# Kernel optimization log

Measured on AMD Instinct MI355X. Metric: run time of the kernel, lower is better.

## Reference

```python
import jax, jax.numpy as jnp
import numpy as np

N = 100000   # active voxels
K = 27       # 3x3x3 kernel offsets
C = 64       # in_channels == out_channels (residual block)
EPS = 1e-5


def setup_inputs() -> dict:
    key = jax.random.key(0)
    ks = jax.random.split(key, 10)
    feats = jax.random.normal(ks[0], (N, C), dtype=jnp.float32)
    # kernel-map: for each voxel, index of the neighbor voxel for each of the 27 offsets
    nbr = jax.random.randint(ks[1], (N, K), 0, N)
    nbr = nbr.at[:, K // 2].set(jnp.arange(N))  # center offset is identity
    w_scale = 1.0 / np.sqrt(K * C)
    W1 = jax.random.normal(ks[2], (K, C, C), dtype=jnp.float32) * w_scale
    b1 = jax.random.normal(ks[3], (C,), dtype=jnp.float32) * 0.01
    g1 = jnp.ones((C,), jnp.float32)
    be1 = jnp.zeros((C,), jnp.float32)
    W2 = jax.random.normal(ks[4], (K, C, C), dtype=jnp.float32) * w_scale
    b2 = jax.random.normal(ks[5], (C,), dtype=jnp.float32) * 0.01
    g2 = jnp.ones((C,), jnp.float32)
    be2 = jnp.zeros((C,), jnp.float32)
    return {"feats": feats, "nbr": nbr, "W1": W1, "b1": b1, "g1": g1, "be1": be1,
            "W2": W2, "b2": b2, "g2": g2, "be2": be2}


def _sparse_conv(f, nbr, W, b):
    # gather neighbor features per kernel offset: [N, K, C]
    g = f[nbr]
    # per-offset matmul and reduce over offsets (gather-matmul-scatter form)
    return jnp.einsum('nkc,kcd->nd', g, W) + b


def _bn(x, gamma, beta):
    # BatchNorm over active voxels (training-mode batch stats, per channel)
    mu = x.mean(axis=0)
    var = x.var(axis=0)
    return (x - mu) * jax.lax.rsqrt(var + EPS) * gamma + beta


def reference(feats, nbr, W1, b1, g1, be1, W2, b2, g2, be2):
    h = jax.nn.relu(_bn(_sparse_conv(feats, nbr, W1, b1), g1, be1))
    h = _bn(_sparse_conv(h, nbr, W2, b2), g2, be2)
    return jax.nn.relu(h + feats)  # residual add + ReLU
```

## Files before the change

### kernel.cpp

```cpp
#include <hip/hip_runtime.h>

#define NCH 64
#define KOFF 27
#define EPSV 1e-5f

typedef __attribute__((ext_vector_type(8))) short  bf16x8;
typedef __attribute__((ext_vector_type(4))) float  f32x4;
typedef __attribute__((ext_vector_type(8))) unsigned short u16x8;

__device__ __forceinline__ unsigned short f2bf(float x) {
    unsigned int u = __float_as_uint(x);
    u += 0x7fffu + ((u >> 16) & 1u);
    return (unsigned short)(u >> 16);
}

__global__ __launch_bounds__(256)
void prep_kernel(const float* __restrict__ feats,
                 const float* __restrict__ W1, const float* __restrict__ W2,
                 unsigned short* __restrict__ fbf,
                 unsigned short* __restrict__ wt1, unsigned short* __restrict__ wt2,
                 float* __restrict__ stat, int total8)
{
    const int b = blockIdx.x;
    if (b == 0) {
        stat[threadIdx.x] = 0.f;
        return;
    }
    if (b <= 108) {
        const float* W = (b <= 54) ? W1 : W2;
        unsigned short* Wt = (b <= 54) ? wt1 : wt2;
        const int t = (b <= 54 ? b - 1 : b - 55) * 256 + threadIdx.x;
        const int l  = t & 63;
        const int ct = (t >> 6) & 3;
        const int s  = (t >> 8) & 1;
        const int k  = t >> 9;
        const int d     = ct * 16 + (l & 15);
        const int cbase = s * 32 + (l >> 4) * 8;
        u16x8 o;
#pragma unroll
        for (int j = 0; j < 8; ++j)
            o[j] = f2bf(W[(size_t)k * 4096 + (size_t)(cbase + j) * 64 + d]);
        reinterpret_cast<u16x8*>(Wt)[t] = o;
        return;
    }
    const int idx = (b - 109) * 256 + threadIdx.x;
    if (idx >= total8) return;
    const float4* xp = reinterpret_cast<const float4*>(feats) + (size_t)idx * 2;
    const float4 a = xp[0], c = xp[1];
    u16x8 o;
    o[0] = f2bf(a.x); o[1] = f2bf(a.y); o[2] = f2bf(a.z); o[3] = f2bf(a.w);
    o[4] = f2bf(c.x); o[5] = f2bf(c.y); o[6] = f2bf(c.z); o[7] = f2bf(c.w);
    reinterpret_cast<u16x8*>(fbf)[idx] = o;
}

__global__ __launch_bounds__(128, 4)
void conv_mfma_kernel(const unsigned short* __restrict__ fin,
                      const int* __restrict__ nbr,
                      const unsigned short* __restrict__ Wt,
                      const float* __restrict__ bias,
                      float* __restrict__ out, float* __restrict__ pstat, int N)
{
    __shared__ int   s_idx[32 * KOFF];
    __shared__ f32x4 s_comb4[8][64];

    const int lane = threadIdx.x & 63;
    const int wv   = threadIdx.x >> 6;
    const int n0   = blockIdx.x * 32;
    const int m    = lane & 15;
    const int quad = lane >> 4;

    {
        const int rem  = N - n0;
        const int maxi = (rem < 32 ? rem : 32) * KOFF;
        const int* nb  = nbr + (size_t)n0 * KOFF;
        for (int p = threadIdx.x; p < 32 * KOFF; p += 128)
            s_idx[p] = ((p < maxi) ? nb[p] : 0) * (NCH * 2);
    }
    __syncthreads();

    f32x4 acc[2][4];
#pragma unroll
    for (int mt = 0; mt < 2; ++mt)
#pragma unroll
        for (int ct = 0; ct < 4; ++ct) acc[mt][ct] = (f32x4){0.f, 0.f, 0.f, 0.f};

    bf16x8 A[2][2][2];
    bf16x8 B[2][4];
    const char* finB = (const char*)fin;

#define LOADA(kk, p)                                                         \
    {                                                                        \
        _Pragma("unroll")                                                    \
        for (int mt = 0; mt < 2; ++mt) {                                     \
            const int ofs = s_idx[(mt * 16 + m) * KOFF + (kk)];              \
            const char* fp = finB + ofs + quad * 16;                         \
            A[p][mt][0] = *reinterpret_cast<const bf16x8*>(fp);              \
            A[p][mt][1] = *reinterpret_cast<const bf16x8*>(fp + 64);         \
        }                                                                    \
    }

#define LOADB(kk)                                                            \
    {                                                                        \
        const unsigned short* wp = Wt + (size_t)(kk) * 4096 + lane * 8;      \
        _Pragma("unroll")                                                    \
        for (int s = 0; s < 2; ++s)                                          \
            _Pragma("unroll")                                                \
            for (int ct = 0; ct < 4; ++ct)                                   \
                B[s][ct] =                                                   \
                    *reinterpret_cast<const bf16x8*>(wp + (s * 4 + ct) * 512);\
    }

#define DOMFMA(p)                                                            \
    {                                                                        \
        _Pragma("unroll")                                                    \
        for (int mt = 0; mt < 2; ++mt)                                       \
            _Pragma("unroll")                                                \
            for (int s = 0; s < 2; ++s)                                      \
                _Pragma("unroll")                                            \
                for (int ct = 0; ct < 4; ++ct)                               \
                    acc[mt][ct] = __builtin_amdgcn_mfma_f32_16x16x32_bf16(   \
                        A[p][mt][s], B[s][ct], acc[mt][ct], 0, 0, 0);        \
    }

    const int kbeg = wv ? 14 : 0;
    const int kend = wv ? KOFF : 14;
    LOADA(kbeg, 0);
    int k = kbeg;
#pragma unroll 1
    for (; k + 2 < kend; k += 2) {
        LOADB(k);
        LOADA(k + 1, 1);
        __builtin_amdgcn_sched_barrier(0);
        DOMFMA(0);
        LOADB(k + 1);
        LOADA(k + 2, 0);
        __builtin_amdgcn_sched_barrier(0);
        DOMFMA(1);
    }
    if (k + 1 < kend) {
        LOADB(k);
        LOADA(k + 1, 1);
        __builtin_amdgcn_sched_barrier(0);
        DOMFMA(0);
        LOADB(k + 1);
        DOMFMA(1);
    } else {
        LOADB(k);
        DOMFMA(0);
    }
#undef LOADA
#undef LOADB
#undef DOMFMA

    if (wv == 1) {
#pragma unroll
        for (int mt = 0; mt < 2; ++mt)
#pragma unroll
            for (int ct = 0; ct < 4; ++ct)
                s_comb4[mt * 4 + ct][lane] = acc[mt][ct];
    }
    __syncthreads();
    if (wv == 0) {
#pragma unroll
        for (int ct = 0; ct < 4; ++ct) {
            const int ch = ct * 16 + m;
            const float bv = bias[ch];
            float s = 0.f, q = 0.f;
#pragma unroll
            for (int mt = 0; mt < 2; ++mt) {
                const f32x4 part = s_comb4[mt * 4 + ct][lane];
#pragma unroll
                for (int r = 0; r < 4; ++r) {
                    const int vox = n0 + mt * 16 + quad * 4 + r;
                    if (vox < N) {
                        const float v = acc[mt][ct][r] + part[r] + bv;
                        out[(size_t)vox * NCH + ch] = v;
                        s += v;
                        q += v * v;
                    }
                }
            }
            s += __shfl_xor(s, 16, 64);
            s += __shfl_xor(s, 32, 64);
            q += __shfl_xor(q, 16, 64);
            q += __shfl_xor(q, 32, 64);
            if (quad == 0) {
                float* pr = pstat + (size_t)blockIdx.x * 128;
                pr[ch]      = s;
                pr[64 + ch] = q;
            }
        }
    }
}

__global__ __launch_bounds__(256)
void reduce_stats_kernel(const float* __restrict__ pstat, float* __restrict__ stat,
                         int rows)
{
    __shared__ float s_[256];
    const int ch = threadIdx.x & 127;
    const int h  = threadIdx.x >> 7;
    float acc = 0.f;
    for (int r = blockIdx.x * 2 + h; r < rows; r += gridDim.x * 2)
        acc += pstat[(size_t)r * 128 + ch];
    s_[threadIdx.x] = acc;
    __syncthreads();
    if (threadIdx.x < 128)
        atomicAdd(&stat[threadIdx.x], s_[threadIdx.x] + s_[threadIdx.x + 128]);
}

__global__ __launch_bounds__(256)
void bn_relu_bf16_kernel(const float* __restrict__ x, const float* __restrict__ sums,
                         const float* __restrict__ gmm, const float* __restrict__ bet,
                         float invN, unsigned short* __restrict__ y, int total8)
{
    const int idx = blockIdx.x * 256 + threadIdx.x;
    if (idx >= total8) return;
    const int c0 = (idx & 7) * 8;
    const float4* xp = reinterpret_cast<const float4*>(x) + (size_t)idx * 2;
    const float4 a = xp[0], b = xp[1];
    float v[8] = {a.x, a.y, a.z, a.w, b.x, b.y, b.z, b.w};
    u16x8 o;
#pragma unroll
    for (int i = 0; i < 8; ++i) {
        const int c = c0 + i;
        const float mu  = sums[c] * invN;
        const float var = sums[64 + c] * invN - mu * mu;
        const float rs  = rsqrtf(var + EPSV);
        const float sc  = gmm[c] * rs;
        const float sh  = bet[c] - mu * sc;
        o[i] = f2bf(fmaxf(fmaf(v[i], sc, sh), 0.f));
    }
    reinterpret_cast<u16x8*>(y)[idx] = o;
}

__global__ __launch_bounds__(256)
void bn_res_relu_kernel(float* __restrict__ x, const float* __restrict__ feats,
                        const float* __restrict__ sums, const float* __restrict__ gmm,
                        const float* __restrict__ bet, float invN, int total4)
{
    const int idx = blockIdx.x * blockDim.x + threadIdx.x;
    if (idx >= total4) return;
    float4 v = reinterpret_cast<float4*>(x)[idx];
    const float4 f = reinterpret_cast<const float4*>(feats)[idx];
    const int c0 = (idx & 15) * 4;
    float sc[4], sh[4];
#pragma unroll
    for (int i = 0; i < 4; ++i) {
        const int c = c0 + i;
        const float mu  = sums[c] * invN;
        const float var = sums[64 + c] * invN - mu * mu;
        const float rs  = rsqrtf(var + EPSV);
        sc[i] = gmm[c] * rs;
        sh[i] = bet[c] - mu * sc[i];
    }
    v.x = fmaxf(fmaf(v.x, sc[0], sh[0]) + f.x, 0.f);
    v.y = fmaxf(fmaf(v.y, sc[1], sh[1]) + f.y, 0.f);
    v.z = fmaxf(fmaf(v.z, sc[2], sh[2]) + f.z, 0.f);
    v.w = fmaxf(fmaf(v.w, sc[3], sh[3]) + f.w, 0.f);
    reinterpret_cast<float4*>(x)[idx] = v;
}

extern "C" void kernel_launch(void* const* d_in, const int* in_sizes, int n_in,
                              void* d_out, int out_size, void* d_ws, size_t ws_size,
                              hipStream_t stream)
{
    const float* feats = (const float*)d_in[0];
    const int*   nbr   = (const int*)d_in[1];
    const float* W1    = (const float*)d_in[2];
    const float* b1    = (const float*)d_in[3];
    const float* g1    = (const float*)d_in[4];
    const float* be1   = (const float*)d_in[5];
    const float* W2    = (const float*)d_in[6];
    const float* b2    = (const float*)d_in[7];
    const float* g2    = (const float*)d_in[8];
    const float* be2   = (const float*)d_in[9];
    float* out = (float*)d_out;

    const int N  = in_sizes[0] / NCH;
    const int NC = N * NCH;
    const float invN = 1.0f / (float)N;

    float*          h0   = (float*)d_ws;
    unsigned short* fbf  = (unsigned short*)(h0 + NC);
    unsigned short* hbf  = fbf + NC;
    unsigned short* wt1  = hbf + NC;
    unsigned short* wt2  = wt1 + KOFF * 4096;
    float*          stat = (float*)(wt2 + KOFF * 4096);

    const int total8   = NC / 8;
    const int castGrid = (total8 + 255) / 256;
    const int prepGrid = 1 + 108 + castGrid;
    const int convGrid = (N + 31) / 32;

    float* pstat1 = out;
    float* pstat2 = h0;

    prep_kernel<<<prepGrid, 256, 0, stream>>>(feats, W1, W2, fbf, wt1, wt2,
                                              stat, total8);
    conv_mfma_kernel<<<convGrid, 128, 0, stream>>>(fbf, nbr, wt1, b1, h0,
                                                   pstat1, N);
    reduce_stats_kernel<<<32, 256, 0, stream>>>(pstat1, stat, convGrid);
    bn_relu_bf16_kernel<<<castGrid, 256, 0, stream>>>(h0, stat, g1, be1, invN,
                                                      hbf, total8);
    conv_mfma_kernel<<<convGrid, 128, 0, stream>>>(hbf, nbr, wt2, b2, out,
                                                   pstat2, N);
    reduce_stats_kernel<<<32, 256, 0, stream>>>(pstat2, stat + 128, convGrid);
    bn_res_relu_kernel<<<(NC / 4 + 255) / 256, 256, 0, stream>>>(
        out, feats, stat + 128, g2, be2, invN, NC / 4);
}
```

Before: 292.0 us.

## Stage conv weights in LDS and widen blocks to 128 voxels

The conv kernel now runs 4 waves per block, each owning 32 voxels across all 27 offsets, instead of 2 waves splitting the offsets for 32 voxels. Weights are staged into shared memory in chunks of 6 offsets, so all waves share them rather than each reading them from global memory. This also removes the cross-wave partial-sum combine through LDS. In exchange it adds block-wide barriers per chunk, a larger LDS footprint (about 62 KB) that limits occupancy, and more stat rows for the reduce kernel.

```diff
diff --git a/kernel.cpp b/kernel.cpp
--- a/kernel.cpp
+++ b/kernel.cpp
@@ -53,30 +53,29 @@
     reinterpret_cast<u16x8*>(fbf)[idx] = o;
 }
 
-__global__ __launch_bounds__(128, 4)
+__global__ __launch_bounds__(256, 2)
 void conv_mfma_kernel(const unsigned short* __restrict__ fin,
                       const int* __restrict__ nbr,
                       const unsigned short* __restrict__ Wt,
                       const float* __restrict__ bias,
                       float* __restrict__ out, float* __restrict__ pstat, int N)
 {
-    __shared__ int   s_idx[32 * KOFF];
-    __shared__ f32x4 s_comb4[8][64];
+    __shared__ int            s_idx[128 * KOFF];
+    __shared__ unsigned short s_w[6 * 4096];
 
     const int lane = threadIdx.x & 63;
     const int wv   = threadIdx.x >> 6;
-    const int n0   = blockIdx.x * 32;
+    const int n0   = blockIdx.x * 128;
     const int m    = lane & 15;
     const int quad = lane >> 4;
 
     {
         const int rem  = N - n0;
-        const int maxi = (rem < 32 ? rem : 32) * KOFF;
+        const int maxi = (rem < 128 ? rem : 128) * KOFF;
         const int* nb  = nbr + (size_t)n0 * KOFF;
-        for (int p = threadIdx.x; p < 32 * KOFF; p += 128)
+        for (int p = threadIdx.x; p < 128 * KOFF; p += 256)
             s_idx[p] = ((p < maxi) ? nb[p] : 0) * (NCH * 2);
     }
-    __syncthreads();
 
     f32x4 acc[2][4];
 #pragma unroll
@@ -87,21 +86,22 @@
     bf16x8 A[2][2][2];
     bf16x8 B[2][4];
     const char* finB = (const char*)fin;
+    const int lv0 = wv * 32;
 
 #define LOADA(kk, p)                                                         \
     {                                                                        \
         _Pragma("unroll")                                                    \
         for (int mt = 0; mt < 2; ++mt) {                                     \
-            const int ofs = s_idx[(mt * 16 + m) * KOFF + (kk)];              \
+            const int ofs = s_idx[(lv0 + mt * 16 + m) * KOFF + (kk)];        \
             const char* fp = finB + ofs + quad * 16;                         \
             A[p][mt][0] = *reinterpret_cast<const bf16x8*>(fp);              \
             A[p][mt][1] = *reinterpret_cast<const bf16x8*>(fp + 64);         \
         }                                                                    \
     }
 
-#define LOADB(kk)                                                            \
+#define LOADB_LDS(kk)                                                        \
     {                                                                        \
-        const unsigned short* wp = Wt + (size_t)(kk) * 4096 + lane * 8;      \
+        const unsigned short* wp = s_w + (kk) * 4096 + lane * 8;             \
         _Pragma("unroll")                                                    \
         for (int s = 0; s < 2; ++s)                                          \
             _Pragma("unroll")                                                \
@@ -122,73 +122,82 @@
                         A[p][mt][s], B[s][ct], acc[mt][ct], 0, 0, 0);        \
     }
 
-    const int kbeg = wv ? 14 : 0;
-    const int kend = wv ? KOFF : 14;
-    LOADA(kbeg, 0);
-    int k = kbeg;
 #pragma unroll 1
-    for (; k + 2 < kend; k += 2) {
-        LOADB(k);
-        LOADA(k + 1, 1);
-        __builtin_amdgcn_sched_barrier(0);
-        DOMFMA(0);
-        LOADB(k + 1);
-        LOADA(k + 2, 0);
-        __builtin_amdgcn_sched_barrier(0);
-        DOMFMA(1);
-    }
-    if (k + 1 < kend) {
-        LOADB(k);
-        LOADA(k + 1, 1);
-        __builtin_amdgcn_sched_barrier(0);
-        DOMFMA(0);
-        LOADB(k + 1);
-        DOMFMA(1);
-    } else {
-        LOADB(k);
-        DOMFMA(0);
+    for (int c = 0; c < 5; ++c) {
+        const int kb  = c * 6;
+        const int len = (KOFF - kb < 6) ? (KOFF - kb) : 6;
+
+        {
+            const u16x8* gw = reinterpret_cast<const u16x8*>(
+                Wt + (size_t)kb * 4096);
+            u16x8* lw = reinterpret_cast<u16x8*>(s_w);
+            const int units = len * 512;
+#pragma unroll
+            for (int i = 0; i < 12; ++i) {
+                const int u = threadIdx.x + i * 256;
+                if (u < units) lw[u] = gw[u];
+            }
+        }
+        LOADA(kb, 0);
+        __syncthreads();
+
+        int kk = 0;
+#pragma unroll 1
+        for (; kk + 2 < len; kk += 2) {
+            LOADA(kb + kk + 1, 1);
+            LOADB_LDS(kk);
+            __builtin_amdgcn_sched_barrier(0);
+            DOMFMA(0);
+            LOADA(kb + kk + 2, 0);
+            LOADB_LDS(kk + 1);
+            __builtin_amdgcn_sched_barrier(0);
+            DOMFMA(1);
+        }
+        if (kk + 1 < len) {
+            LOADA(kb + kk + 1, 1);
+            LOADB_LDS(kk);
+            __builtin_amdgcn_sched_barrier(0);
+            DOMFMA(0);
+            LOADB_LDS(kk + 1);
+            __builtin_amdgcn_sched_barrier(0);
+            DOMFMA(1);
+        } else {
+            LOADB_LDS(kk);
+            __builtin_amdgcn_sched_barrier(0);
+            DOMFMA(0);
+        }
+        __syncthreads();
     }
 #undef LOADA
-#undef LOADB
+#undef LOADB_LDS
 #undef DOMFMA
 
-    if (wv == 1) {
-#pragma unroll
-        for (int mt = 0; mt < 2; ++mt)
-#pragma unroll
-            for (int ct = 0; ct < 4; ++ct)
-                s_comb4[mt * 4 + ct][lane] = acc[mt][ct];
-    }
-    __syncthreads();
-    if (wv == 0) {
-#pragma unroll
-        for (int ct = 0; ct < 4; ++ct) {
-            const int ch = ct * 16 + m;
-            const float bv = bias[ch];
-            float s = 0.f, q = 0.f;
-#pragma unroll
-            for (int mt = 0; mt < 2; ++mt) {
-                const f32x4 part = s_comb4[mt * 4 + ct][lane];
-#pragma unroll
-                for (int r = 0; r < 4; ++r) {
-                    const int vox = n0 + mt * 16 + quad * 4 + r;
-                    if (vox < N) {
-                        const float v = acc[mt][ct][r] + part[r] + bv;
-                        out[(size_t)vox * NCH + ch] = v;
-                        s += v;
-                        q += v * v;
-                    }
+#pragma unroll
+    for (int ct = 0; ct < 4; ++ct) {
+        const int ch = ct * 16 + m;
+        const float bv = bias[ch];
+        float s = 0.f, q = 0.f;
+#pragma unroll
+        for (int mt = 0; mt < 2; ++mt) {
+#pragma unroll
+            for (int r = 0; r < 4; ++r) {
+                const int vox = n0 + lv0 + mt * 16 + quad * 4 + r;
+                if (vox < N) {
+                    const float v = acc[mt][ct][r] + bv;
+                    out[(size_t)vox * NCH + ch] = v;
+                    s += v;
+                    q += v * v;
                 }
             }
-            s += __shfl_xor(s, 16, 64);
-            s += __shfl_xor(s, 32, 64);
-            q += __shfl_xor(q, 16, 64);
-            q += __shfl_xor(q, 32, 64);
-            if (quad == 0) {
-                float* pr = pstat + (size_t)blockIdx.x * 128;
-                pr[ch]      = s;
-                pr[64 + ch] = q;
-            }
+        }
+        s += __shfl_xor(s, 16, 64);
+        s += __shfl_xor(s, 32, 64);
+        q += __shfl_xor(q, 16, 64);
+        q += __shfl_xor(q, 32, 64);
+        if (quad == 0) {
+            float* pr = pstat + ((size_t)blockIdx.x * 4 + wv) * 128;
+            pr[ch]      = s;
+            pr[64 + ch] = q;
         }
     }
 }
@@ -291,21 +300,22 @@
     const int total8   = NC / 8;
     const int castGrid = (total8 + 255) / 256;
     const int prepGrid = 1 + 108 + castGrid;
-    const int convGrid = (N + 31) / 32;
+    const int convGrid = (N + 127) / 128;
+    const int statRows = convGrid * 4;
 
     float* pstat1 = out;
     float* pstat2 = h0;
 
     prep_kernel<<<prepGrid, 256, 0, stream>>>(feats, W1, W2, fbf, wt1, wt2,
                                               stat, total8);
-    conv_mfma_kernel<<<convGrid, 128, 0, stream>>>(fbf, nbr, wt1, b1, h0,
+    conv_mfma_kernel<<<convGrid, 256, 0, stream>>>(fbf, nbr, wt1, b1, h0,
                                                    pstat1, N);
-    reduce_stats_kernel<<<32, 256, 0, stream>>>(pstat1, stat, convGrid);
+    reduce_stats_kernel<<<32, 256, 0, stream>>>(pstat1, stat, statRows);
     bn_relu_bf16_kernel<<<castGrid, 256, 0, stream>>>(h0, stat, g1, be1, invN,
                                                       hbf, total8);
-    conv_mfma_kernel<<<convGrid, 128, 0, stream>>>(hbf, nbr, wt2, b2, out,
+    conv_mfma_kernel<<<convGrid, 256, 0, stream>>>(hbf, nbr, wt2, b2, out,
                                                    pstat2, N);
-    reduce_stats_kernel<<<32, 256, 0, stream>>>(pstat2, stat + 128, convGrid);
+    reduce_stats_kernel<<<32, 256, 0, stream>>>(pstat2, stat + 128, statRows);
     bn_res_relu_kernel<<<(NC / 4 + 255) / 256, 256, 0, stream>>>(
         out, feats, stat + 128, g2, be2, invN, NC / 4);
 }
```

Result: slower. 326.4 us (+11.8%).
